# Performance work log

Measured on AMD Instinct MI355X. Metric: run time of the kernel, lower is better.

The kernel has to match this reference:

```python
import jax, jax.numpy as jnp
import numpy as np

N = 50000
E = 800000
IN_DIM = 128
HID = 64
HEADS = 4
OUT = 64


def _bn(x, g, b, eps=1e-5):
    # BatchNorm1d with batch statistics (biased var), as in train-mode normalization
    mu = x.mean(0)
    var = ((x - mu) ** 2).mean(0)
    return (x - mu) * jax.lax.rsqrt(var + eps) * g + b


def _gat(x, W, a_src, a_dst, bias, src, dst, heads, dim, concat):
    # PyG GATConv: h = xW; e_ij = LeakyReLU(a_src.h_j + a_dst.h_i); softmax over incoming edges of i
    n = x.shape[0]
    h = (x @ W).reshape(n, heads, dim)            # [N,H,D]
    es = (h * a_src).sum(-1)                      # [N,H]
    ed = (h * a_dst).sum(-1)                      # [N,H]
    e = jax.nn.leaky_relu(es[src] + ed[dst], 0.2)  # [E,H]
    emax = jax.ops.segment_max(e, dst, num_segments=n)
    w = jnp.exp(e - emax[dst])
    denom = jax.ops.segment_sum(w, dst, num_segments=n)
    alpha = w / (denom[dst] + 1e-16)              # [E,H]
    out = jax.ops.segment_sum(h[src] * alpha[:, :, None], dst, num_segments=n)  # [N,H,D]
    out = out.reshape(n, heads * dim) if concat else out.mean(axis=1)
    return out + bias


def _gcn(x, W, bias, src, dst):
    # PyG GCNConv with self-loops (already appended): D^{-1/2} A D^{-1/2} x W
    n = x.shape[0]
    h = x @ W
    deg = jax.ops.segment_sum(jnp.ones(src.shape[0], h.dtype), dst, num_segments=n)
    dinv = jax.lax.rsqrt(jnp.maximum(deg, 1e-12))
    norm = dinv[src] * dinv[dst]                  # [E]
    return jax.ops.segment_sum(h[src] * norm[:, None], dst, num_segments=n) + bias


def setup_inputs() -> dict:
    key = jax.random.key(0)
    ks = jax.random.split(key, 16)
    s = 0.1
    inp = {
        "x": jax.random.normal(ks[0], (N, IN_DIM), jnp.float32),
        "edge_index": jax.random.randint(ks[1], (2, E), 0, N, jnp.int64 if jax.config.jax_enable_x64 else jnp.int32),
        "edge_attr": jax.random.normal(ks[2], (E,), jnp.float32),
        # GAT layer 1
        "W1": jax.random.normal(ks[3], (IN_DIM, HEADS * HID), jnp.float32) * s,
        "att_src1": jax.random.normal(ks[4], (HEADS, HID), jnp.float32) * s,
        "att_dst1": jax.random.normal(ks[5], (HEADS, HID), jnp.float32) * s,
        "b1": jnp.zeros((HEADS * HID,), jnp.float32),
        "g1": jnp.ones((HEADS * HID,), jnp.float32),
        "beta1": jnp.zeros((HEADS * HID,), jnp.float32),
        # GCN
        "Wg": jax.random.normal(ks[6], (HEADS * HID, HID), jnp.float32) * s,
        "bg": jnp.zeros((HID,), jnp.float32),
        "g2": jnp.ones((HID,), jnp.float32),
        "beta2": jnp.zeros((HID,), jnp.float32),
        # GAT layer 2 (heads=1, concat=False)
        "W2": jax.random.normal(ks[7], (HID, OUT), jnp.float32) * s,
        "att_src2": jax.random.normal(ks[8], (1, OUT), jnp.float32) * s,
        "att_dst2": jax.random.normal(ks[9], (1, OUT), jnp.float32) * s,
        "b2": jnp.zeros((OUT,), jnp.float32),
        "g3": jnp.ones((OUT,), jnp.float32),
        "beta3": jnp.zeros((OUT,), jnp.float32),
        # projector
        "Wp1": jax.random.normal(ks[10], (OUT, 128), jnp.float32) * s,
        "bp1": jnp.zeros((128,), jnp.float32),
        "Wp2": jax.random.normal(ks[11], (128, 64), jnp.float32) * s,
        "bp2": jnp.zeros((64,), jnp.float32),
    }
    return inp


def reference(x, edge_index, edge_attr, W1, att_src1, att_dst1, b1, g1, beta1,
              Wg, bg, g2, beta2, W2, att_src2, att_dst2, b2, g3, beta3,
              Wp1, bp1, Wp2, bp2):
    # edge_attr is ignored by GATConv when edge_dim is None (PyG behavior)
    loop = jnp.arange(N, dtype=edge_index.dtype)
    src = jnp.concatenate([edge_index[0], loop])  # self-loops appended
    dst = jnp.concatenate([edge_index[1], loop])
    h = _gat(x, W1, att_src1, att_dst1, b1, src, dst, HEADS, HID, True)
    h = jax.nn.elu(_bn(h, g1, beta1))
    h = _gcn(h, Wg, bg, src, dst)
    h = jax.nn.relu(_bn(h, g2, beta2))
    h = _gat(h, W2, att_src2, att_dst2, b2, src, dst, 1, OUT, False)
    h = jax.nn.elu(_bn(h, g3, beta3))
    return jax.nn.relu(h @ Wp1 + bp1) @ Wp2 + bp2
```

## Files before the change

kernel.cpp:

```cpp
#include <hip/hip_runtime.h>
#include <math.h>

#define NN 50000
#define EE 800000
#define E2 850000
#define SCB 196

__device__ __forceinline__ float bf2f(unsigned short u) {
  return __uint_as_float(((unsigned int)u) << 16);
}
__device__ __forceinline__ unsigned short f2bf(float f) {
  unsigned int x = __float_as_uint(f);
  unsigned int r = (x + 0x7fffu + ((x >> 16) & 1u)) >> 16;
  return (unsigned short)r;
}

__device__ __forceinline__ float leaky(float x) { return x > 0.f ? x : 0.2f * x; }

__device__ __forceinline__ int edge_src(const int* ei, int e) {
  return (e < EE) ? ei[e] : (e - EE);
}
__device__ __forceinline__ int edge_dst(const int* ei, int e) {
  return (e < EE) ? ei[EE + e] : (e - EE);
}

__global__ void k_deg(const int* __restrict__ ei, int* __restrict__ deg) {
  int e = blockIdx.x * blockDim.x + threadIdx.x;
  if (e < E2) atomicAdd(&deg[edge_dst(ei, e)], 1);
}

__global__ __launch_bounds__(256) void k_scan1(const int* __restrict__ deg,
                                               int* __restrict__ partial) {
  __shared__ int sd[256];
  int i = blockIdx.x * 256 + threadIdx.x;
  sd[threadIdx.x] = (i < NN) ? deg[i] : 0;
  __syncthreads();
  for (int off = 128; off > 0; off >>= 1) {
    if (threadIdx.x < off) sd[threadIdx.x] += sd[threadIdx.x + off];
    __syncthreads();
  }
  if (threadIdx.x == 0) partial[blockIdx.x] = sd[0];
}

__global__ __launch_bounds__(256) void k_scan2(int* __restrict__ partial) {
  __shared__ int sd[256];
  int t = threadIdx.x;
  int orig = (t < SCB) ? partial[t] : 0;
  sd[t] = orig;
  __syncthreads();
  for (int off = 1; off < 256; off <<= 1) {
    int v = (t >= off) ? sd[t - off] : 0;
    __syncthreads();
    sd[t] += v;
    __syncthreads();
  }
  if (t < SCB) partial[t] = sd[t] - orig;
}

__global__ __launch_bounds__(256) void k_scan3(const int* __restrict__ deg,
                                               const int* __restrict__ partial,
                                               int* __restrict__ rowptr,
                                               int* __restrict__ cnt,
                                               float* __restrict__ dinv) {
  __shared__ int sd[256];
  int t = threadIdx.x;
  int i = blockIdx.x * 256 + t;
  int v = (i < NN) ? deg[i] : 0;
  sd[t] = v;
  __syncthreads();
  for (int off = 1; off < 256; off <<= 1) {
    int u = (t >= off) ? sd[t - off] : 0;
    __syncthreads();
    sd[t] += u;
    __syncthreads();
  }
  if (i < NN) {
    int excl = partial[blockIdx.x] + sd[t] - v;
    rowptr[i] = excl;
    cnt[i] = excl;
    dinv[i] = rsqrtf((float)v);
  }
  if (i == 0) rowptr[NN] = E2;
}

__global__ void k_fill(const int* __restrict__ ei, int* __restrict__ cnt,
                       int* __restrict__ csr) {
  int e = blockIdx.x * blockDim.x + threadIdx.x;
  if (e >= E2) return;
  int d = edge_dst(ei, e);
  int s = edge_src(ei, e);
  int pos = atomicAdd(&cnt[d], 1);
  csr[pos] = s;
}

__global__ __launch_bounds__(256) void k_gemm(
    const float* __restrict__ A, const unsigned short* __restrict__ Abf,
    const float* __restrict__ B, const float* __restrict__ biasOut,
    const float* __restrict__ bnst, const float* __restrict__ bng,
    const float* __restrict__ bnb, int inAct, int outAct,
    float* __restrict__ Cf, unsigned short* __restrict__ Cbf,
    const float* __restrict__ rowScale,
    int M, int K, int NC) {
  __shared__ float As[64][68];
  __shared__ float Bs[64][68];
  __shared__ float sSc[256], sSh[256];
  int tx = threadIdx.x & 15;
  int ty = threadIdx.x >> 4;
  if (bnst) {
    int c = threadIdx.x;
    if (c < K) {
      float sum = 0.f, sq = 0.f;
      for (int cp = 0; cp < 32; ++cp) {
        sum += bnst[cp * 2 * K + c];
        sq += bnst[cp * 2 * K + K + c];
      }
      const float invN = 1.0f / (float)NN;
      float mu = sum * invN;
      float var = sq * invN - mu * mu;
      float rs = rsqrtf(var + 1e-5f);
      float sc = rs * bng[c];
      sSc[c] = sc;
      sSh[c] = fmaf(-mu, sc, bnb[c]);
    }
    __syncthreads();
  }
  int rowBase = blockIdx.x * 64;
  int colBase = blockIdx.y * 64;
  float acc[4][4];
#pragma unroll
  for (int i = 0; i < 4; ++i)
#pragma unroll
    for (int j = 0; j < 4; ++j) acc[i][j] = 0.f;

  for (int kc = 0; kc < K; kc += 64) {
#pragma unroll
    for (int l = 0; l < 4; ++l) {
      int r = ty + l * 16;
      int gr = rowBase + r;
      float4 av = make_float4(0.f, 0.f, 0.f, 0.f);
      if (gr < M) {
        if (Abf) {
          ushort4 u4 = *(const ushort4*)&Abf[(size_t)gr * K + kc + tx * 4];
          av = make_float4(bf2f(u4.x), bf2f(u4.y), bf2f(u4.z), bf2f(u4.w));
        } else {
          av = *(const float4*)&A[(size_t)gr * K + kc + tx * 4];
        }
      }
      if (bnst) {
        int c = kc + tx * 4;
        av.x = fmaf(av.x, sSc[c + 0], sSh[c + 0]);
        av.y = fmaf(av.y, sSc[c + 1], sSh[c + 1]);
        av.z = fmaf(av.z, sSc[c + 2], sSh[c + 2]);
        av.w = fmaf(av.w, sSc[c + 3], sSh[c + 3]);
      }
      if (inAct == 1) {
        av.x = fmaxf(av.x, 0.f); av.y = fmaxf(av.y, 0.f);
        av.z = fmaxf(av.z, 0.f); av.w = fmaxf(av.w, 0.f);
      } else if (inAct == 2) {
        av.x = av.x > 0.f ? av.x : expm1f(av.x);
        av.y = av.y > 0.f ? av.y : expm1f(av.y);
        av.z = av.z > 0.f ? av.z : expm1f(av.z);
        av.w = av.w > 0.f ? av.w : expm1f(av.w);
      }
      As[tx * 4 + 0][r] = av.x;
      As[tx * 4 + 1][r] = av.y;
      As[tx * 4 + 2][r] = av.z;
      As[tx * 4 + 3][r] = av.w;
      float4 bv = *(const float4*)&B[(size_t)(kc + r) * NC + colBase + tx * 4];
      *(float4*)&Bs[r][tx * 4] = bv;
    }
    __syncthreads();
#pragma unroll
    for (int kk = 0; kk < 64; ++kk) {
      float4 av = *(const float4*)&As[kk][ty * 4];
      float4 bv = *(const float4*)&Bs[kk][tx * 4];
      float a_[4] = {av.x, av.y, av.z, av.w};
      float b_[4] = {bv.x, bv.y, bv.z, bv.w};
#pragma unroll
      for (int i = 0; i < 4; ++i)
#pragma unroll
        for (int j = 0; j < 4; ++j) acc[i][j] = fmaf(a_[i], b_[j], acc[i][j]);
    }
    __syncthreads();
  }

  float4 bb = make_float4(0.f, 0.f, 0.f, 0.f);
  if (biasOut) bb = *(const float4*)&biasOut[colBase + tx * 4];
#pragma unroll
  for (int i = 0; i < 4; ++i) {
    int gr = rowBase + ty * 4 + i;
    if (gr < M) {
      float4 v;
      v.x = acc[i][0] + bb.x;
      v.y = acc[i][1] + bb.y;
      v.z = acc[i][2] + bb.z;
      v.w = acc[i][3] + bb.w;
      if (outAct == 1) {
        v.x = fmaxf(v.x, 0.f); v.y = fmaxf(v.y, 0.f);
        v.z = fmaxf(v.z, 0.f); v.w = fmaxf(v.w, 0.f);
      }
      if (Cf) *(float4*)&Cf[(size_t)gr * NC + colBase + tx * 4] = v;
      if (Cbf) {
        float rs_ = rowScale ? rowScale[gr] : 1.f;
        ushort4 u;
        u.x = f2bf(v.x * rs_); u.y = f2bf(v.y * rs_);
        u.z = f2bf(v.z * rs_); u.w = f2bf(v.w * rs_);
        *(ushort4*)&Cbf[(size_t)gr * NC + colBase + tx * 4] = u;
      }
    }
  }
}

__global__ void k_dots1(const unsigned short* __restrict__ h1b,
                        const float* __restrict__ a_src, const float* __restrict__ a_dst,
                        float* __restrict__ es, float* __restrict__ ed) {
  int wave = threadIdx.x >> 6;
  int lane = threadIdx.x & 63;
  int i = blockIdx.x * 4 + wave;
  if (i >= NN) return;
  ushort4 hv4 = *(const ushort4*)&h1b[(size_t)i * 256 + lane * 4];
  float4 hv = make_float4(bf2f(hv4.x), bf2f(hv4.y), bf2f(hv4.z), bf2f(hv4.w));
  float4 as = *(const float4*)&a_src[lane * 4];
  float4 ad = *(const float4*)&a_dst[lane * 4];
  float ps = hv.x * as.x + hv.y * as.y + hv.z * as.z + hv.w * as.w;
  float pd = hv.x * ad.x + hv.y * ad.y + hv.z * ad.z + hv.w * ad.w;
#pragma unroll
  for (int off = 8; off > 0; off >>= 1) {
    ps += __shfl_xor(ps, off);
    pd += __shfl_xor(pd, off);
  }
  if ((lane & 15) == 0) {
    int h = lane >> 4;
    es[i * 4 + h] = ps;
    ed[i * 4 + h] = pd;
  }
}

__global__ void k_dots2(const unsigned short* __restrict__ h2b,
                        const float* __restrict__ a_src, const float* __restrict__ a_dst,
                        float* __restrict__ es, float* __restrict__ ed) {
  int wave = threadIdx.x >> 6;
  int lane = threadIdx.x & 63;
  int i = blockIdx.x * 4 + wave;
  if (i >= NN) return;
  float h = bf2f(h2b[(size_t)i * 64 + lane]);
  float ps = h * a_src[lane];
  float pd = h * a_dst[lane];
#pragma unroll
  for (int off = 32; off > 0; off >>= 1) {
    ps += __shfl_xor(ps, off);
    pd += __shfl_xor(pd, off);
  }
  if (lane == 0) { es[i] = ps; ed[i] = pd; }
}

__global__ __launch_bounds__(256) void k_soft1(const float* __restrict__ es,
                                               const float* __restrict__ ed,
                                               const int* __restrict__ rowptr,
                                               const int* __restrict__ csr,
                                               float* __restrict__ w1) {
  int node = blockIdx.x * 16 + (threadIdx.x >> 4);
  int sub = threadIdx.x & 15;
  int start = rowptr[node], end = rowptr[node + 1];
  float4 edv = *(const float4*)&ed[node * 4];
  float m0 = -1e30f, m1 = -1e30f, m2 = -1e30f, m3 = -1e30f;
  float s0 = 0.f, s1 = 0.f, s2 = 0.f, s3 = 0.f;
  for (int k = start + sub; k < end; k += 16) {
    int s = csr[k];
    float4 esv = *(const float4*)&es[s * 4];
    float e0 = leaky(esv.x + edv.x);
    float e1 = leaky(esv.y + edv.y);
    float e2 = leaky(esv.z + edv.z);
    float e3 = leaky(esv.w + edv.w);
    float mn;
    mn = fmaxf(m0, e0); s0 = s0 * __expf(m0 - mn) + __expf(e0 - mn); m0 = mn;
    mn = fmaxf(m1, e1); s1 = s1 * __expf(m1 - mn) + __expf(e1 - mn); m1 = mn;
    mn = fmaxf(m2, e2); s2 = s2 * __expf(m2 - mn) + __expf(e2 - mn); m2 = mn;
    mn = fmaxf(m3, e3); s3 = s3 * __expf(m3 - mn) + __expf(e3 - mn); m3 = mn;
  }
#pragma unroll
  for (int off = 1; off < 16; off <<= 1) {
    float mo, so, mn;
    mo = __shfl_xor(m0, off); so = __shfl_xor(s0, off);
    mn = fmaxf(m0, mo); s0 = s0 * __expf(m0 - mn) + so * __expf(mo - mn); m0 = mn;
    mo = __shfl_xor(m1, off); so = __shfl_xor(s1, off);
    mn = fmaxf(m1, mo); s1 = s1 * __expf(m1 - mn) + so * __expf(mo - mn); m1 = mn;
    mo = __shfl_xor(m2, off); so = __shfl_xor(s2, off);
    mn = fmaxf(m2, mo); s2 = s2 * __expf(m2 - mn) + so * __expf(mo - mn); m2 = mn;
    mo = __shfl_xor(m3, off); so = __shfl_xor(s3, off);
    mn = fmaxf(m3, mo); s3 = s3 * __expf(m3 - mn) + so * __expf(mo - mn); m3 = mn;
  }
  float i0 = 1.f / (s0 + 1e-16f);
  float i1 = 1.f / (s1 + 1e-16f);
  float i2 = 1.f / (s2 + 1e-16f);
  float i3 = 1.f / (s3 + 1e-16f);
  for (int k = start + sub; k < end; k += 16) {
    int s = csr[k];
    float4 esv = *(const float4*)&es[s * 4];
    w1[k]          = __expf(leaky(esv.x + edv.x) - m0) * i0;
    w1[E2 + k]     = __expf(leaky(esv.y + edv.y) - m1) * i1;
    w1[2 * E2 + k] = __expf(leaky(esv.z + edv.z) - m2) * i2;
    w1[3 * E2 + k] = __expf(leaky(esv.w + edv.w) - m3) * i3;
  }
}

__global__ __launch_bounds__(256) void k_soft2(const float* __restrict__ es,
                                               const float* __restrict__ ed,
                                               const int* __restrict__ rowptr,
                                               const int* __restrict__ csr,
                                               float* __restrict__ w2) {
  int node = blockIdx.x * 16 + (threadIdx.x >> 4);
  int sub = threadIdx.x & 15;
  int start = rowptr[node], end = rowptr[node + 1];
  float edi = ed[node];
  float m = -1e30f, ss = 0.f;
  for (int k = start + sub; k < end; k += 16) {
    float e = leaky(es[csr[k]] + edi);
    float mn = fmaxf(m, e);
    ss = ss * __expf(m - mn) + __expf(e - mn);
    m = mn;
  }
#pragma unroll
  for (int off = 1; off < 16; off <<= 1) {
    float mo = __shfl_xor(m, off);
    float so = __shfl_xor(ss, off);
    float mn = fmaxf(m, mo);
    ss = ss * __expf(m - mn) + so * __expf(mo - mn);
    m = mn;
  }
  float inv = 1.f / (ss + 1e-16f);
  for (int k = start + sub; k < end; k += 16) {
    float e = leaky(es[csr[k]] + edi);
    w2[k] = __expf(e - m) * inv;
  }
}

__global__ __launch_bounds__(256) void k_gat1(const unsigned short* __restrict__ h1b,
                                              const float* __restrict__ w1,
                                              const int* __restrict__ rowptr,
                                              const int* __restrict__ csr,
                                              const float* __restrict__ b1,
                                              unsigned short* __restrict__ outb,
                                              float* __restrict__ st) {
  __shared__ float2 sm[4][256];
  int wave = threadIdx.x >> 6;
  int lane = threadIdx.x & 63;
  int i = blockIdx.x * 4 + wave;
  int start = rowptr[i], end = rowptr[i + 1];
  const float* wh = w1 + (size_t)(lane >> 4) * E2;
  float4 acc = make_float4(0.f, 0.f, 0.f, 0.f);
  int k = start;
  for (; k + 4 <= end; k += 4) {
    int sA = csr[k], sB = csr[k + 1], sC = csr[k + 2], sD = csr[k + 3];
    float wA = wh[k], wB = wh[k + 1], wC = wh[k + 2], wD = wh[k + 3];
    ushort4 a0 = *(const ushort4*)&h1b[(size_t)sA * 256 + lane * 4];
    ushort4 a1 = *(const ushort4*)&h1b[(size_t)sB * 256 + lane * 4];
    ushort4 a2 = *(const ushort4*)&h1b[(size_t)sC * 256 + lane * 4];
    ushort4 a3 = *(const ushort4*)&h1b[(size_t)sD * 256 + lane * 4];
    acc.x = fmaf(bf2f(a0.x), wA, fmaf(bf2f(a1.x), wB, fmaf(bf2f(a2.x), wC, fmaf(bf2f(a3.x), wD, acc.x))));
    acc.y = fmaf(bf2f(a0.y), wA, fmaf(bf2f(a1.y), wB, fmaf(bf2f(a2.y), wC, fmaf(bf2f(a3.y), wD, acc.y))));
    acc.z = fmaf(bf2f(a0.z), wA, fmaf(bf2f(a1.z), wB, fmaf(bf2f(a2.z), wC, fmaf(bf2f(a3.z), wD, acc.z))));
    acc.w = fmaf(bf2f(a0.w), wA, fmaf(bf2f(a1.w), wB, fmaf(bf2f(a2.w), wC, fmaf(bf2f(a3.w), wD, acc.w))));
  }
  for (; k < end; ++k) {
    int s = csr[k];
    float wv = wh[k];
    ushort4 a0 = *(const ushort4*)&h1b[(size_t)s * 256 + lane * 4];
    acc.x = fmaf(bf2f(a0.x), wv, acc.x);
    acc.y = fmaf(bf2f(a0.y), wv, acc.y);
    acc.z = fmaf(bf2f(a0.z), wv, acc.z);
    acc.w = fmaf(bf2f(a0.w), wv, acc.w);
  }
  float4 bv = *(const float4*)&b1[lane * 4];
  float4 o;
  o.x = acc.x + bv.x; o.y = acc.y + bv.y; o.z = acc.z + bv.z; o.w = acc.w + bv.w;
  ushort4 u;
  u.x = f2bf(o.x); u.y = f2bf(o.y); u.z = f2bf(o.z); u.w = f2bf(o.w);
  *(ushort4*)&outb[(size_t)i * 256 + lane * 4] = u;
  sm[wave][lane * 4 + 0] = make_float2(o.x, o.x * o.x);
  sm[wave][lane * 4 + 1] = make_float2(o.y, o.y * o.y);
  sm[wave][lane * 4 + 2] = make_float2(o.z, o.z * o.z);
  sm[wave][lane * 4 + 3] = make_float2(o.w, o.w * o.w);
  __syncthreads();
  int c = threadIdx.x;
  float s_ = 0.f, q_ = 0.f;
#pragma unroll
  for (int wv = 0; wv < 4; ++wv) { float2 v = sm[wv][c]; s_ += v.x; q_ += v.y; }
  float* dst = st + (size_t)(blockIdx.x & 31) * 512;
  atomicAdd(&dst[c], s_);
  atomicAdd(&dst[256 + c], q_);
}

__global__ __launch_bounds__(256) void k_gcn(const unsigned short* __restrict__ hgb,
                                             const float* __restrict__ dinv,
                                             const int* __restrict__ rowptr,
                                             const int* __restrict__ csr,
                                             const float* __restrict__ bg,
                                             float* __restrict__ out,
                                             float* __restrict__ st) {
  __shared__ float2 sm[4][64];
  int wave = threadIdx.x >> 6;
  int lane = threadIdx.x & 63;
  int i = blockIdx.x * 4 + wave;
  int start = rowptr[i], end = rowptr[i + 1];
  float acc = 0.f;
  int k = start;
  for (; k + 4 <= end; k += 4) {
    int sA = csr[k], sB = csr[k + 1], sC = csr[k + 2], sD = csr[k + 3];
    acc += bf2f(hgb[(size_t)sA * 64 + lane]) + bf2f(hgb[(size_t)sB * 64 + lane]) +
           bf2f(hgb[(size_t)sC * 64 + lane]) + bf2f(hgb[(size_t)sD * 64 + lane]);
  }
  for (; k < end; ++k) acc += bf2f(hgb[(size_t)csr[k] * 64 + lane]);
  float o = fmaf(acc, dinv[i], bg[lane]);
  out[(size_t)i * 64 + lane] = o;
  sm[wave][lane] = make_float2(o, o * o);
  __syncthreads();
  if (threadIdx.x < 64) {
    int c = threadIdx.x;
    float s_ = 0.f, q_ = 0.f;
#pragma unroll
    for (int wv = 0; wv < 4; ++wv) { float2 v = sm[wv][c]; s_ += v.x; q_ += v.y; }
    float* dst = st + (size_t)(blockIdx.x & 31) * 128;
    atomicAdd(&dst[c], s_);
    atomicAdd(&dst[64 + c], q_);
  }
}

__global__ __launch_bounds__(256) void k_gat2(const unsigned short* __restrict__ h2b,
                                              const float* __restrict__ w2,
                                              const int* __restrict__ rowptr,
                                              const int* __restrict__ csr,
                                              const float* __restrict__ b2,
                                              float* __restrict__ out,
                                              float* __restrict__ st) {
  __shared__ float2 sm[4][64];
  int wave = threadIdx.x >> 6;
  int lane = threadIdx.x & 63;
  int i = blockIdx.x * 4 + wave;
  int start = rowptr[i], end = rowptr[i + 1];
  float acc = 0.f;
  int k = start;
  for (; k + 4 <= end; k += 4) {
    int sA = csr[k], sB = csr[k + 1], sC = csr[k + 2], sD = csr[k + 3];
    float wA = w2[k], wB = w2[k + 1], wC = w2[k + 2], wD = w2[k + 3];
    acc = fmaf(bf2f(h2b[(size_t)sA * 64 + lane]), wA,
          fmaf(bf2f(h2b[(size_t)sB * 64 + lane]), wB,
          fmaf(bf2f(h2b[(size_t)sC * 64 + lane]), wC,
          fmaf(bf2f(h2b[(size_t)sD * 64 + lane]), wD, acc))));
  }
  for (; k < end; ++k)
    acc = fmaf(bf2f(h2b[(size_t)csr[k] * 64 + lane]), w2[k], acc);
  float o = acc + b2[lane];
  out[(size_t)i * 64 + lane] = o;
  sm[wave][lane] = make_float2(o, o * o);
  __syncthreads();
  if (threadIdx.x < 64) {
    int c = threadIdx.x;
    float s_ = 0.f, q_ = 0.f;
#pragma unroll
    for (int wv = 0; wv < 4; ++wv) { float2 v = sm[wv][c]; s_ += v.x; q_ += v.y; }
    float* dst = st + (size_t)(blockIdx.x & 31) * 128;
    atomicAdd(&dst[c], s_);
    atomicAdd(&dst[64 + c], q_);
  }
}

extern "C" void kernel_launch(void* const* d_in, const int* in_sizes, int n_in,
                              void* d_out, int out_size, void* d_ws, size_t ws_size,
                              hipStream_t stream) {
  const float* x        = (const float*)d_in[0];
  const int*   ei       = (const int*)d_in[1];
  const float* W1       = (const float*)d_in[3];
  const float* att_src1 = (const float*)d_in[4];
  const float* att_dst1 = (const float*)d_in[5];
  const float* b1       = (const float*)d_in[6];
  const float* g1       = (const float*)d_in[7];
  const float* beta1    = (const float*)d_in[8];
  const float* Wg       = (const float*)d_in[9];
  const float* bg       = (const float*)d_in[10];
  const float* g2       = (const float*)d_in[11];
  const float* beta2    = (const float*)d_in[12];
  const float* W2       = (const float*)d_in[13];
  const float* att_src2 = (const float*)d_in[14];
  const float* att_dst2 = (const float*)d_in[15];
  const float* b2       = (const float*)d_in[16];
  const float* g3       = (const float*)d_in[17];
  const float* beta3    = (const float*)d_in[18];
  const float* Wp1      = (const float*)d_in[19];
  const float* bp1      = (const float*)d_in[20];
  const float* Wp2      = (const float*)d_in[21];
  const float* bp2      = (const float*)d_in[22];
  float* out = (float*)d_out;

  char* w = (char*)d_ws;
  unsigned short* bufBb  = (unsigned short*)(w + 0);
  float*          bufD   = (float*)(w + 0);
  unsigned short* h1b    = (unsigned short*)(w + 51200000);
  float*          hidden = (float*)(w + 51200000);
  float*          w1     = (float*)(w + 76800000);
  float*          w2     = (float*)(w + 76800000);
  unsigned short* hgb    = (unsigned short*)(w + 90400000);
  float*          bufC   = (float*)(w + 96800000);
  unsigned short* h2b    = (unsigned short*)(w + 109600000);
  float*          es1    = (float*)(w + 116000000);
  float*          ed1    = (float*)(w + 116800000);
  float*          es2    = (float*)(w + 117600000);
  float*          ed2    = (float*)(w + 117800000);
  float*          dinv   = (float*)(w + 118000000);
  int*            deg    = (int*)(w + 118200000);
  int*            rowptr = (int*)(w + 118400000);
  int*            cnt    = (int*)(w + 118600064);
  int*            csr    = (int*)(w + 118800064);
  float*          st1    = (float*)(w + 122200064);
  float*          st2    = st1 + 32 * 512;
  float*          st3    = st2 + 32 * 128;
  int*            partial= (int*)(st3 + 32 * 128);

  hipMemsetAsync(deg, 0, NN * sizeof(int), stream);
  hipMemsetAsync(st1, 0, (32 * 512 + 32 * 128 + 32 * 128) * sizeof(float), stream);

  const int EB = (E2 + 255) / 256;
  const int WB = NN / 4;
  const int SB = NN / 16;
  const int GX = (NN + 63) / 64;

  k_deg<<<EB, 256, 0, stream>>>(ei, deg);
  k_scan1<<<SCB, 256, 0, stream>>>(deg, partial);
  k_scan2<<<1, 256, 0, stream>>>(partial);
  k_scan3<<<SCB, 256, 0, stream>>>(deg, partial, rowptr, cnt, dinv);
  k_fill<<<EB, 256, 0, stream>>>(ei, cnt, csr);

  k_gemm<<<dim3(GX, 4), 256, 0, stream>>>(x, nullptr, W1, nullptr, nullptr, nullptr,
                                          nullptr, 0, 0, nullptr, h1b, nullptr, NN, 128, 256);
  k_dots1<<<WB, 256, 0, stream>>>(h1b, att_src1, att_dst1, es1, ed1);
  k_soft1<<<SB, 256, 0, stream>>>(es1, ed1, rowptr, csr, w1);
  k_gat1<<<WB, 256, 0, stream>>>(h1b, w1, rowptr, csr, b1, bufBb, st1);

  k_gemm<<<dim3(GX, 1), 256, 0, stream>>>(nullptr, bufBb, Wg, nullptr, st1, g1,
                                          beta1, 2, 0, nullptr, hgb, dinv, NN, 256, 64);
  k_gcn<<<WB, 256, 0, stream>>>(hgb, dinv, rowptr, csr, bg, bufC, st2);

  k_gemm<<<dim3(GX, 1), 256, 0, stream>>>(bufC, nullptr, W2, nullptr, st2, g2,
                                          beta2, 1, 0, nullptr, h2b, nullptr, NN, 64, 64);
  k_dots2<<<WB, 256, 0, stream>>>(h2b, att_src2, att_dst2, es2, ed2);
  k_soft2<<<SB, 256, 0, stream>>>(es2, ed2, rowptr, csr, w2);
  k_gat2<<<WB, 256, 0, stream>>>(h2b, w2, rowptr, csr, b2, bufD, st3);

  k_gemm<<<dim3(GX, 2), 256, 0, stream>>>(bufD, nullptr, Wp1, bp1, st3, g3,
                                          beta3, 2, 1, hidden, nullptr, nullptr, NN, 64, 128);
  k_gemm<<<dim3(GX, 1), 256, 0, stream>>>(hidden, nullptr, Wp2, bp2, nullptr, nullptr,
                                          nullptr, 0, 0, out, nullptr, nullptr, NN, 128, 64);
}
```

Baseline: 542.2 us.

## Fuse attention dots into GEMM epilogue, enlarge GEMM tile, merge scan kernels

Attention source/destination dot products are now computed in the GEMM epilogue, so the separate k_dots1/k_dots2 kernels and their re-read of the bf16 features go away. The GEMM tile changes from 64x64 with K-step 64 to 128x64 with K-step 32, giving each thread 8x4 outputs. The single-block k_scan2 is folded into k_scan3, where every block redundantly scans the partial sums. The GAT1 stats shared-memory layout is also split into separate sum and square arrays. The epilogue dot products use fp32 values before bf16 rounding, so results differ slightly from the old path, and the larger tile adds register pressure.

```diff
diff --git a/kernel.cpp b/kernel.cpp
--- a/kernel.cpp
+++ b/kernel.cpp
@@ -5,6 +5,7 @@
 #define EE 800000
 #define E2 850000
 #define SCB 196
+#define GXL 391
 
 __device__ __forceinline__ float bf2f(unsigned short u) {
   return __uint_as_float(((unsigned int)u) << 16);
@@ -42,28 +43,23 @@
   if (threadIdx.x == 0) partial[blockIdx.x] = sd[0];
 }
 
-__global__ __launch_bounds__(256) void k_scan2(int* __restrict__ partial) {
-  __shared__ int sd[256];
-  int t = threadIdx.x;
-  int orig = (t < SCB) ? partial[t] : 0;
-  sd[t] = orig;
-  __syncthreads();
-  for (int off = 1; off < 256; off <<= 1) {
-    int v = (t >= off) ? sd[t - off] : 0;
-    __syncthreads();
-    sd[t] += v;
-    __syncthreads();
-  }
-  if (t < SCB) partial[t] = sd[t] - orig;
-}
-
 __global__ __launch_bounds__(256) void k_scan3(const int* __restrict__ deg,
                                                const int* __restrict__ partial,
                                                int* __restrict__ rowptr,
                                                int* __restrict__ cnt,
                                                float* __restrict__ dinv) {
+  __shared__ int sp[256];
   __shared__ int sd[256];
   int t = threadIdx.x;
+  sp[t] = (t < SCB) ? partial[t] : 0;
+  __syncthreads();
+  for (int off = 1; off < 256; off <<= 1) {
+    int v = (t >= off) ? sp[t - off] : 0;
+    __syncthreads();
+    sp[t] += v;
+    __syncthreads();
+  }
+  int base = (blockIdx.x == 0) ? 0 : sp[blockIdx.x - 1];
   int i = blockIdx.x * 256 + t;
   int v = (i < NN) ? deg[i] : 0;
   sd[t] = v;
@@ -75,7 +71,7 @@
     __syncthreads();
   }
   if (i < NN) {
-    int excl = partial[blockIdx.x] + sd[t] - v;
+    int excl = base + sd[t] - v;
     rowptr[i] = excl;
     cnt[i] = excl;
     dinv[i] = rsqrtf((float)v);
@@ -100,14 +96,16 @@
     const float* __restrict__ bnb, int inAct, int outAct,
     float* __restrict__ Cf, unsigned short* __restrict__ Cbf,
     const float* __restrict__ rowScale,
+    const float* __restrict__ attSrc, const float* __restrict__ attDst,
+    float* __restrict__ esOut, float* __restrict__ edOut, int attMode,
     int M, int K, int NC) {
-  __shared__ float As[64][68];
-  __shared__ float Bs[64][68];
+  __shared__ float As[32][132];
+  __shared__ float Bs[32][68];
   __shared__ float sSc[256], sSh[256];
-  int tx = threadIdx.x & 15;
-  int ty = threadIdx.x >> 4;
+  int t = threadIdx.x;
+  int tx = t & 15, ty = t >> 4;
   if (bnst) {
-    int c = threadIdx.x;
+    int c = t;
     if (c < K) {
       float sum = 0.f, sq = 0.f;
       for (int cp = 0; cp < 32; ++cp) {
@@ -124,30 +122,32 @@
     }
     __syncthreads();
   }
-  int rowBase = blockIdx.x * 64;
+  int rowBase = blockIdx.x * 128;
   int colBase = blockIdx.y * 64;
-  float acc[4][4];
-#pragma unroll
-  for (int i = 0; i < 4; ++i)
+  float acc[8][4];
+#pragma unroll
+  for (int i = 0; i < 8; ++i)
 #pragma unroll
     for (int j = 0; j < 4; ++j) acc[i][j] = 0.f;
 
-  for (int kc = 0; kc < K; kc += 64) {
-#pragma unroll
-    for (int l = 0; l < 4; ++l) {
-      int r = ty + l * 16;
-      int gr = rowBase + r;
+  int kq = t & 7;
+  int r0 = t >> 3;
+  for (int kc = 0; kc < K; kc += 32) {
+#pragma unroll
+    for (int i2 = 0; i2 < 4; ++i2) {
+      int row = r0 + 32 * i2;
+      int gr = rowBase + row;
       float4 av = make_float4(0.f, 0.f, 0.f, 0.f);
       if (gr < M) {
         if (Abf) {
-          ushort4 u4 = *(const ushort4*)&Abf[(size_t)gr * K + kc + tx * 4];
+          ushort4 u4 = *(const ushort4*)&Abf[(size_t)gr * K + kc + kq * 4];
           av = make_float4(bf2f(u4.x), bf2f(u4.y), bf2f(u4.z), bf2f(u4.w));
         } else {
-          av = *(const float4*)&A[(size_t)gr * K + kc + tx * 4];
+          av = *(const float4*)&A[(size_t)gr * K + kc + kq * 4];
         }
       }
       if (bnst) {
-        int c = kc + tx * 4;
+        int c = kc + kq * 4;
         av.x = fmaf(av.x, sSc[c + 0], sSh[c + 0]);
         av.y = fmaf(av.y, sSc[c + 1], sSh[c + 1]);
         av.z = fmaf(av.z, sSc[c + 2], sSh[c + 2]);
@@ -162,22 +162,28 @@
         av.z = av.z > 0.f ? av.z : expm1f(av.z);
         av.w = av.w > 0.f ? av.w : expm1f(av.w);
       }
-      As[tx * 4 + 0][r] = av.x;
-      As[tx * 4 + 1][r] = av.y;
-      As[tx * 4 + 2][r] = av.z;
-      As[tx * 4 + 3][r] = av.w;
-      float4 bv = *(const float4*)&B[(size_t)(kc + r) * NC + colBase + tx * 4];
-      *(float4*)&Bs[r][tx * 4] = bv;
+      As[kq * 4 + 0][row] = av.x;
+      As[kq * 4 + 1][row] = av.y;
+      As[kq * 4 + 2][row] = av.z;
+      As[kq * 4 + 3][row] = av.w;
     }
-    __syncthreads();
-#pragma unroll
-    for (int kk = 0; kk < 64; ++kk) {
-      float4 av = *(const float4*)&As[kk][ty * 4];
+#pragma unroll
+    for (int i2 = 0; i2 < 2; ++i2) {
+      int u = t + 256 * i2;
+      int c4 = u & 15, kk = u >> 4;
+      float4 bv = *(const float4*)&B[(size_t)(kc + kk) * NC + colBase + c4 * 4];
+      *(float4*)&Bs[kk][c4 * 4] = bv;
+    }
+    __syncthreads();
+#pragma unroll
+    for (int kk = 0; kk < 32; ++kk) {
+      float4 a0 = *(const float4*)&As[kk][ty * 8];
+      float4 a1 = *(const float4*)&As[kk][ty * 8 + 4];
       float4 bv = *(const float4*)&Bs[kk][tx * 4];
-      float a_[4] = {av.x, av.y, av.z, av.w};
+      float a_[8] = {a0.x, a0.y, a0.z, a0.w, a1.x, a1.y, a1.z, a1.w};
       float b_[4] = {bv.x, bv.y, bv.z, bv.w};
 #pragma unroll
-      for (int i = 0; i < 4; ++i)
+      for (int i = 0; i < 8; ++i)
 #pragma unroll
         for (int j = 0; j < 4; ++j) acc[i][j] = fmaf(a_[i], b_[j], acc[i][j]);
     }
@@ -186,9 +192,14 @@
 
   float4 bb = make_float4(0.f, 0.f, 0.f, 0.f);
   if (biasOut) bb = *(const float4*)&biasOut[colBase + tx * 4];
-#pragma unroll
-  for (int i = 0; i < 4; ++i) {
-    int gr = rowBase + ty * 4 + i;
+  float4 as4 = make_float4(0.f, 0.f, 0.f, 0.f), ad4 = as4;
+  if (attMode) {
+    as4 = *(const float4*)&attSrc[colBase + tx * 4];
+    ad4 = *(const float4*)&attDst[colBase + tx * 4];
+  }
+#pragma unroll
+  for (int i = 0; i < 8; ++i) {
+    int gr = rowBase + ty * 8 + i;
     if (gr < M) {
       float4 v;
       v.x = acc[i][0] + bb.x;
@@ -207,51 +218,26 @@
         u.z = f2bf(v.z * rs_); u.w = f2bf(v.w * rs_);
         *(ushort4*)&Cbf[(size_t)gr * NC + colBase + tx * 4] = u;
       }
+      if (attMode) {
+        float pes = v.x * as4.x + v.y * as4.y + v.z * as4.z + v.w * as4.w;
+        float ped = v.x * ad4.x + v.y * ad4.y + v.z * ad4.z + v.w * ad4.w;
+#pragma unroll
+        for (int off = 8; off > 0; off >>= 1) {
+          pes += __shfl_xor(pes, off);
+          ped += __shfl_xor(ped, off);
+        }
+        if (tx == 0) {
+          if (attMode == 1) {
+            esOut[gr * 4 + blockIdx.y] = pes;
+            edOut[gr * 4 + blockIdx.y] = ped;
+          } else {
+            esOut[gr] = pes;
+            edOut[gr] = ped;
+          }
+        }
+      }
     }
   }
-}
-
-__global__ void k_dots1(const unsigned short* __restrict__ h1b,
-                        const float* __restrict__ a_src, const float* __restrict__ a_dst,
-                        float* __restrict__ es, float* __restrict__ ed) {
-  int wave = threadIdx.x >> 6;
-  int lane = threadIdx.x & 63;
-  int i = blockIdx.x * 4 + wave;
-  if (i >= NN) return;
-  ushort4 hv4 = *(const ushort4*)&h1b[(size_t)i * 256 + lane * 4];
-  float4 hv = make_float4(bf2f(hv4.x), bf2f(hv4.y), bf2f(hv4.z), bf2f(hv4.w));
-  float4 as = *(const float4*)&a_src[lane * 4];
-  float4 ad = *(const float4*)&a_dst[lane * 4];
-  float ps = hv.x * as.x + hv.y * as.y + hv.z * as.z + hv.w * as.w;
-  float pd = hv.x * ad.x + hv.y * ad.y + hv.z * ad.z + hv.w * ad.w;
-#pragma unroll
-  for (int off = 8; off > 0; off >>= 1) {
-    ps += __shfl_xor(ps, off);
-    pd += __shfl_xor(pd, off);
-  }
-  if ((lane & 15) == 0) {
-    int h = lane >> 4;
-    es[i * 4 + h] = ps;
-    ed[i * 4 + h] = pd;
-  }
-}
-
-__global__ void k_dots2(const unsigned short* __restrict__ h2b,
-                        const float* __restrict__ a_src, const float* __restrict__ a_dst,
-                        float* __restrict__ es, float* __restrict__ ed) {
-  int wave = threadIdx.x >> 6;
-  int lane = threadIdx.x & 63;
-  int i = blockIdx.x * 4 + wave;
-  if (i >= NN) return;
-  float h = bf2f(h2b[(size_t)i * 64 + lane]);
-  float ps = h * a_src[lane];
-  float pd = h * a_dst[lane];
-#pragma unroll
-  for (int off = 32; off > 0; off >>= 1) {
-    ps += __shfl_xor(ps, off);
-    pd += __shfl_xor(pd, off);
-  }
-  if (lane == 0) { es[i] = ps; ed[i] = pd; }
 }
 
 __global__ __launch_bounds__(256) void k_soft1(const float* __restrict__ es,
@@ -342,7 +328,8 @@
                                               const float* __restrict__ b1,
                                               unsigned short* __restrict__ outb,
                                               float* __restrict__ st) {
-  __shared__ float2 sm[4][256];
+  __shared__ float smS[4][256];
+  __shared__ float smQ[4][256];
   int wave = threadIdx.x >> 6;
   int lane = threadIdx.x & 63;
   int i = blockIdx.x * 4 + wave;
@@ -377,15 +364,14 @@
   ushort4 u;
   u.x = f2bf(o.x); u.y = f2bf(o.y); u.z = f2bf(o.z); u.w = f2bf(o.w);
   *(ushort4*)&outb[(size_t)i * 256 + lane * 4] = u;
-  sm[wave][lane * 4 + 0] = make_float2(o.x, o.x * o.x);
-  sm[wave][lane * 4 + 1] = make_float2(o.y, o.y * o.y);
-  sm[wave][lane * 4 + 2] = make_float2(o.z, o.z * o.z);
-  sm[wave][lane * 4 + 3] = make_float2(o.w, o.w * o.w);
+  *(float4*)&smS[wave][lane * 4] = o;
+  float4 q = make_float4(o.x * o.x, o.y * o.y, o.z * o.z, o.w * o.w);
+  *(float4*)&smQ[wave][lane * 4] = q;
   __syncthreads();
   int c = threadIdx.x;
   float s_ = 0.f, q_ = 0.f;
 #pragma unroll
-  for (int wv = 0; wv < 4; ++wv) { float2 v = sm[wv][c]; s_ += v.x; q_ += v.y; }
+  for (int wv = 0; wv < 4; ++wv) { s_ += smS[wv][c]; q_ += smQ[wv][c]; }
   float* dst = st + (size_t)(blockIdx.x & 31) * 512;
   atomicAdd(&dst[c], s_);
   atomicAdd(&dst[256 + c], q_);
@@ -522,32 +508,43 @@
   const int EB = (E2 + 255) / 256;
   const int WB = NN / 4;
   const int SB = NN / 16;
-  const int GX = (NN + 63) / 64;
 
   k_deg<<<EB, 256, 0, stream>>>(ei, deg);
   k_scan1<<<SCB, 256, 0, stream>>>(deg, partial);
-  k_scan2<<<1, 256, 0, stream>>>(partial);
   k_scan3<<<SCB, 256, 0, stream>>>(deg, partial, rowptr, cnt, dinv);
   k_fill<<<EB, 256, 0, stream>>>(ei, cnt, csr);
 
-  k_gemm<<<dim3(GX, 4), 256, 0, stream>>>(x, nullptr, W1, nullptr, nullptr, nullptr,
-                                          nullptr, 0, 0, nullptr, h1b, nullptr, NN, 128, 256);
-  k_dots1<<<WB, 256, 0, stream>>>(h1b, att_src1, att_dst1, es1, ed1);
+  k_gemm<<<dim3(GXL, 4), 256, 0, stream>>>(x, nullptr, W1, nullptr,
+                                           nullptr, nullptr, nullptr, 0, 0,
+                                           nullptr, h1b, nullptr,
+                                           att_src1, att_dst1, es1, ed1, 1,
+                                           NN, 128, 256);
   k_soft1<<<SB, 256, 0, stream>>>(es1, ed1, rowptr, csr, w1);
   k_gat1<<<WB, 256, 0, stream>>>(h1b, w1, rowptr, csr, b1, bufBb, st1);
 
-  k_gemm<<<dim3(GX, 1), 256, 0, stream>>>(nullptr, bufBb, Wg, nullptr, st1, g1,
-                                          beta1, 2, 0, nullptr, hgb, dinv, NN, 256, 64);
+  k_gemm<<<dim3(GXL, 1), 256, 0, stream>>>(nullptr, bufBb, Wg, nullptr,
+                                           st1, g1, beta1, 2, 0,
+                                           nullptr, hgb, dinv,
+                                           nullptr, nullptr, nullptr, nullptr, 0,
+                                           NN, 256, 64);
   k_gcn<<<WB, 256, 0, stream>>>(hgb, dinv, rowptr, csr, bg, bufC, st2);
 
-  k_gemm<<<dim3(GX, 1), 256, 0, stream>>>(bufC, nullptr, W2, nullptr, st2, g2,
-                                          beta2, 1, 0, nullptr, h2b, nullptr, NN, 64, 64);
-  k_dots2<<<WB, 256, 0, stream>>>(h2b, att_src2, att_dst2, es2, ed2);
+  k_gemm<<<dim3(GXL, 1), 256, 0, stream>>>(bufC, nullptr, W2, nullptr,
+                                           st2, g2, beta2, 1, 0,
+                                           nullptr, h2b, nullptr,
+                                           att_src2, att_dst2, es2, ed2, 2,
+                                           NN, 64, 64);
   k_soft2<<<SB, 256, 0, stream>>>(es2, ed2, rowptr, csr, w2);
   k_gat2<<<WB, 256, 0, stream>>>(h2b, w2, rowptr, csr, b2, bufD, st3);
 
-  k_gemm<<<dim3(GX, 2), 256, 0, stream>>>(bufD, nullptr, Wp1, bp1, st3, g3,
-                                          beta3, 2, 1, hidden, nullptr, nullptr, NN, 64, 128);
-  k_gemm<<<dim3(GX, 1), 256, 0, stream>>>(hidden, nullptr, Wp2, bp2, nullptr, nullptr,
-                                          nullptr, 0, 0, out, nullptr, nullptr, NN, 128, 64);
-}
+  k_gemm<<<dim3(GXL, 2), 256, 0, stream>>>(bufD, nullptr, Wp1, bp1,
+                                           st3, g3, beta3, 2, 1,
+                                           hidden, nullptr, nullptr,
+                                           nullptr, nullptr, nullptr, nullptr, 0,
+                                           NN, 64, 128);
+  k_gemm<<<dim3(GXL, 1), 256, 0, stream>>>(hidden, nullptr, Wp2, bp2,
+                                           nullptr, nullptr, nullptr, 0, 0,
+                                           out, nullptr, nullptr,
+                                           nullptr, nullptr, nullptr, nullptr, 0,
+                                           NN, 128, 64);
+}
```

After: 532.4 us. No clear change (-1.8%).
